# Optimization experiments

Hardware: AMD Instinct MI355X
Metric: run time of the kernel (lower is better)

The kernel has to match this reference:

```python
import jax, jax.numpy as jnp
import numpy as np

N = 1 << 20          # query points
IN_DIMS = 32
HIDDEN = 64
N_INNER = 4          # n_hidden_layers - 1 hidden->hidden layers
OUT_DIMS = 3


def _kaiming(key, shape):
    fan_in = shape[-1]
    bound = np.sqrt(6.0 / fan_in)  # kaiming_uniform with relu gain sqrt(2): sqrt(6/fan_in)
    return jax.random.uniform(key, shape, jnp.float32, -bound, bound)


def setup_inputs() -> dict:
    key = jax.random.key(0)
    ks = jax.random.split(key, 4)
    x = jax.random.normal(ks[0], (N, IN_DIMS), jnp.float32)
    W_in = _kaiming(ks[1], (HIDDEN, IN_DIMS))
    b_in = jnp.zeros((HIDDEN,), jnp.float32)
    W_hid = _kaiming(ks[2], (N_INNER, HIDDEN, HIDDEN))
    b_hid = jnp.zeros((N_INNER, HIDDEN), jnp.float32)
    W_out = _kaiming(ks[3], (OUT_DIMS, HIDDEN))
    b_out = jnp.zeros((OUT_DIMS,), jnp.float32)
    return {"x": x, "W_in": W_in, "b_in": b_in, "W_hid": W_hid,
            "b_hid": b_hid, "W_out": W_out, "b_out": b_out}


def reference(x, W_in, b_in, W_hid, b_hid, W_out, b_out):
    # torch nn.Linear: y = x @ W.T + b
    h = jax.nn.relu(x @ W_in.T + b_in)                     # [N, HIDDEN]

    def step(h, wb):
        W, b = wb
        return jax.nn.relu(h @ W.T + b), None

    h, _ = jax.lax.scan(step, h, (W_hid, b_hid))           # 4 hidden layers
    out = h @ W_out.T + b_out                              # [N, OUT_DIMS]
    return jax.nn.sigmoid(out)                             # output_activation='Sigmoid'
```

## Files before the change

### kernel.cpp

```cpp
#include <hip/hip_runtime.h>
#include <hip/hip_bf16.h>


typedef __attribute__((ext_vector_type(8))) short bf16x8;
typedef __attribute__((ext_vector_type(4))) float f32x4;

#define NFRAG 59
#define IMG_U4 (NFRAG * 64)

__device__ __forceinline__ unsigned cvtpk(float lo, float hi) {
    unsigned r;
    asm("v_cvt_pk_bf16_f32 %0, %1, %2" : "=v"(r) : "v"(lo), "v"(hi));
    return r;
}

__device__ __forceinline__ int pinv(int s) {
    return ((s >> 5) & 1) * 32 + ((s >> 2) & 1) * 16 + ((s >> 3) & 3) * 4 + (s & 3);
}

__device__ uint4 frag_value(int F, int lane,
        const float* __restrict__ W_in,  const float* __restrict__ b_in,
        const float* __restrict__ W_hid, const float* __restrict__ b_hid,
        const float* __restrict__ W_out, const float* __restrict__ b_out) {
    const int j = lane & 15, g = lane >> 4;
    uint4 r = {0u, 0u, 0u, 0u};
    if (F < 4) {
        const float* row = W_in + (F * 16 + j) * 32 + 8 * g;
        r.x = cvtpk(row[0], row[1]); r.y = cvtpk(row[2], row[3]);
        r.z = cvtpk(row[4], row[5]); r.w = cvtpk(row[6], row[7]);
    } else if (F < 36) {
        int q = F - 4, L = q >> 3, nt = (q >> 1) & 3, f = q & 1;
        const float* row = W_hid + (L * 64 + nt * 16 + j) * 64;
        int s0 = 32 * f + 8 * g;
        r.x = cvtpk(row[pinv(s0 + 0)], row[pinv(s0 + 1)]);
        r.y = cvtpk(row[pinv(s0 + 2)], row[pinv(s0 + 3)]);
        r.z = cvtpk(row[pinv(s0 + 4)], row[pinv(s0 + 5)]);
        r.w = cvtpk(row[pinv(s0 + 6)], row[pinv(s0 + 7)]);
    } else if (F < 38) {
        int f = F - 36;
        if (j < 3) {
            const float* row = W_out + j * 64;
            int s0 = 32 * f + 8 * g;
            r.x = cvtpk(row[pinv(s0 + 0)], row[pinv(s0 + 1)]);
            r.y = cvtpk(row[pinv(s0 + 2)], row[pinv(s0 + 3)]);
            r.z = cvtpk(row[pinv(s0 + 4)], row[pinv(s0 + 5)]);
            r.w = cvtpk(row[pinv(s0 + 6)], row[pinv(s0 + 7)]);
        }
    } else {
        union { uint4 u; float f[4]; } t;
        if (F < 42) {
            int nt = F - 38;
#pragma unroll
            for (int rr = 0; rr < 4; ++rr) t.f[rr] = b_in[nt * 16 + 4 * g + rr];
        } else if (F < 58) {
            int q = F - 42, L = q >> 2, nt = q & 3;
#pragma unroll
            for (int rr = 0; rr < 4; ++rr) t.f[rr] = b_hid[L * 64 + nt * 16 + 4 * g + rr];
        } else {
#pragma unroll
            for (int rr = 0; rr < 4; ++rr) t.f[rr] = (4 * g + rr < 3) ? b_out[4 * g + rr] : 0.f;
        }
        r = t.u;
    }
    return r;
}

__global__ void prep_kernel(const float* __restrict__ W_in,  const float* __restrict__ b_in,
                            const float* __restrict__ W_hid, const float* __restrict__ b_hid,
                            const float* __restrict__ W_out, const float* __restrict__ b_out,
                            uint4* __restrict__ img) {
    img[blockIdx.x * 64 + threadIdx.x] =
        frag_value(blockIdx.x, threadIdx.x, W_in, b_in, W_hid, b_hid, W_out, b_out);
}

__device__ __forceinline__ void relu_pack(const f32x4 a[4], bf16x8 h[2]) {
#pragma unroll
    for (int f = 0; f < 2; ++f) {
        union { bf16x8 v; unsigned u[4]; } t;
        t.u[0] = cvtpk(fmaxf(a[2 * f][0], 0.f), fmaxf(a[2 * f][1], 0.f));
        t.u[1] = cvtpk(fmaxf(a[2 * f][2], 0.f), fmaxf(a[2 * f][3], 0.f));
        t.u[2] = cvtpk(fmaxf(a[2 * f + 1][0], 0.f), fmaxf(a[2 * f + 1][1], 0.f));
        t.u[3] = cvtpk(fmaxf(a[2 * f + 1][2], 0.f), fmaxf(a[2 * f + 1][3], 0.f));
        h[f] = t.v;
    }
}

#define MFMA(a, b, c) __builtin_amdgcn_mfma_f32_16x16x32_bf16((a), (b), (c), 0, 0, 0)

template<bool FAST>
__global__ __launch_bounds__(512, 2) void mlp_kernel(
        const float* __restrict__ x, const uint4* __restrict__ img,
        const float* __restrict__ gW_in,  const float* __restrict__ gb_in,
        const float* __restrict__ gW_hid, const float* __restrict__ gb_hid,
        const float* __restrict__ gW_out, const float* __restrict__ gb_out,
        float* __restrict__ out) {
    __shared__ uint4 simg[IMG_U4];
    const int tid = threadIdx.x;

    if (FAST) {
#pragma unroll
        for (int i = 0; i < 8; ++i) {
            int idx = tid + i * 512;
            if (idx < IMG_U4) simg[idx] = img[idx];
        }
    } else {
        for (int idx = tid; idx < IMG_U4; idx += 512)
            simg[idx] = frag_value(idx >> 6, idx & 63,
                                   gW_in, gb_in, gW_hid, gb_hid, gW_out, gb_out);
    }
    __syncthreads();

    const int wave = tid >> 6, lane = tid & 63;
    const int j = lane & 15, g = lane >> 4;
    const uint4* lp = &simg[lane];

    const int base = (blockIdx.x * 8 + wave) * 256;

    f32x4 xrA0, xrA1, xrB0, xrB1;
    {
        const float* p = x + (size_t)(base + j) * 32 + 8 * g;
        xrA0 = *(const f32x4*)p;         xrA1 = *(const f32x4*)(p + 4);
        xrB0 = *(const f32x4*)(p + 512); xrB1 = *(const f32x4*)(p + 516);
    }

#pragma unroll 1
    for (int it = 0; it < 8; ++it) {
        const int p0 = base + it * 32;

        union { bf16x8 v; unsigned u[4]; } xA, xB;
        xA.u[0] = cvtpk(xrA0[0], xrA0[1]); xA.u[1] = cvtpk(xrA0[2], xrA0[3]);
        xA.u[2] = cvtpk(xrA1[0], xrA1[1]); xA.u[3] = cvtpk(xrA1[2], xrA1[3]);
        xB.u[0] = cvtpk(xrB0[0], xrB0[1]); xB.u[1] = cvtpk(xrB0[2], xrB0[3]);
        xB.u[2] = cvtpk(xrB1[0], xrB1[1]); xB.u[3] = cvtpk(xrB1[2], xrB1[3]);

        {
            const int pn = (it < 7) ? p0 + 32 : p0;
            const float* p = x + (size_t)(pn + j) * 32 + 8 * g;
            xrA0 = *(const f32x4*)p;         xrA1 = *(const f32x4*)(p + 4);
            xrB0 = *(const f32x4*)(p + 512); xrB1 = *(const f32x4*)(p + 516);
        }

        f32x4 aA[4], aB[4];
#pragma unroll
        for (int nt = 0; nt < 4; ++nt) {
            bf16x8 w  = *(const bf16x8*)&lp[nt * 64];
            f32x4  bz = *(const f32x4*)&lp[(38 + nt) * 64];
            aA[nt] = MFMA(w, xA.v, bz);
            aB[nt] = MFMA(w, xB.v, bz);
        }
        bf16x8 hA[2], hB[2];
        relu_pack(aA, hA); relu_pack(aB, hB);

#pragma unroll 1
        for (int L = 0; L < 4; ++L) {
            const int wb = (4 + L * 8) * 64;
            const int bb = (42 + L * 4) * 64;
            bf16x8 w0[4], w1[4]; f32x4 bz[4];
#pragma unroll
            for (int nt = 0; nt < 4; ++nt) {
                w0[nt] = *(const bf16x8*)&lp[wb + (2 * nt) * 64];
                w1[nt] = *(const bf16x8*)&lp[wb + (2 * nt + 1) * 64];
                bz[nt] = *(const f32x4*)&lp[bb + nt * 64];
            }
#pragma unroll
            for (int nt = 0; nt < 4; ++nt) {
                aA[nt] = MFMA(w0[nt], hA[0], bz[nt]);
                aB[nt] = MFMA(w0[nt], hB[0], bz[nt]);
            }
#pragma unroll
            for (int nt = 0; nt < 4; ++nt) {
                aA[nt] = MFMA(w1[nt], hA[1], aA[nt]);
                aB[nt] = MFMA(w1[nt], hB[1], aB[nt]);
            }
            relu_pack(aA, hA); relu_pack(aB, hB);
        }

        bf16x8 wo0 = *(const bf16x8*)&lp[36 * 64];
        bf16x8 wo1 = *(const bf16x8*)&lp[37 * 64];
        f32x4  bo  = *(const f32x4*)&lp[58 * 64];
        f32x4 zA = MFMA(wo0, hA[0], bo); zA = MFMA(wo1, hA[1], zA);
        f32x4 zB = MFMA(wo0, hB[0], bo); zB = MFMA(wo1, hB[1], zB);

        if (g == 0) {
            float* oA = out + (size_t)(p0 + j) * 3;
            float* oB = out + (size_t)(p0 + 16 + j) * 3;
#pragma unroll
            for (int r = 0; r < 3; ++r) {
                oA[r] = __builtin_amdgcn_rcpf(1.f + __expf(-zA[r]));
                oB[r] = __builtin_amdgcn_rcpf(1.f + __expf(-zB[r]));
            }
        }
    }
}

extern "C" void kernel_launch(void* const* d_in, const int* in_sizes, int n_in,
                              void* d_out, int out_size, void* d_ws, size_t ws_size,
                              hipStream_t stream) {
    const float* x     = (const float*)d_in[0];
    const float* W_in  = (const float*)d_in[1];
    const float* b_in  = (const float*)d_in[2];
    const float* W_hid = (const float*)d_in[3];
    const float* b_hid = (const float*)d_in[4];
    const float* W_out = (const float*)d_in[5];
    const float* b_out = (const float*)d_in[6];
    float* out = (float*)d_out;

    int n = in_sizes[0] / 32;
    int nblocks = n / 2048;

    if (ws_size >= (size_t)IMG_U4 * 16) {
        hipLaunchKernelGGL(prep_kernel, dim3(NFRAG), dim3(64), 0, stream,
                           W_in, b_in, W_hid, b_hid, W_out, b_out, (uint4*)d_ws);
        hipLaunchKernelGGL((mlp_kernel<true>), dim3(nblocks), dim3(512), 0, stream,
                           x, (const uint4*)d_ws,
                           W_in, b_in, W_hid, b_hid, W_out, b_out, out);
    } else {
        hipLaunchKernelGGL((mlp_kernel<false>), dim3(nblocks), dim3(512), 0, stream,
                           x, (const uint4*)d_ws,
                           W_in, b_in, W_hid, b_hid, W_out, b_out, out);
    }
}
```

Before: 57.02 us.

## Process four 16-point tiles per wave iteration and raise occupancy to four blocks

Each wave now handles 64 points per iteration (four MFMA column tiles) instead of 32, with the hidden-layer loop fully unrolled and processed in pairs. This reuses each loaded weight fragment across more MFMAs and gives more independent MFMA chains to hide latency. The x prefetch for the first tile is issued before the shared-memory barrier, the next tile's prefetch is moved later, and launch bounds now request 4 blocks per CU, which limits registers while the per-thread state has grown. Output stores are packed into 12-byte structs.

```diff
diff --git a/kernel.cpp b/kernel.cpp
--- a/kernel.cpp
+++ b/kernel.cpp
@@ -7,6 +7,8 @@
 
 #define NFRAG 59
 #define IMG_U4 (NFRAG * 64)
+
+struct F3 { float a, b, c; };
 
 __device__ __forceinline__ unsigned cvtpk(float lo, float hi) {
     unsigned r;
@@ -88,7 +90,7 @@
 #define MFMA(a, b, c) __builtin_amdgcn_mfma_f32_16x16x32_bf16((a), (b), (c), 0, 0, 0)
 
 template<bool FAST>
-__global__ __launch_bounds__(512, 2) void mlp_kernel(
+__global__ __launch_bounds__(512, 4) void mlp_kernel(
         const float* __restrict__ x, const uint4* __restrict__ img,
         const float* __restrict__ gW_in,  const float* __restrict__ gb_in,
         const float* __restrict__ gW_hid, const float* __restrict__ gb_hid,
@@ -108,50 +110,55 @@
             simg[idx] = frag_value(idx >> 6, idx & 63,
                                    gW_in, gb_in, gW_hid, gb_hid, gW_out, gb_out);
     }
-    __syncthreads();
 
     const int wave = tid >> 6, lane = tid & 63;
     const int j = lane & 15, g = lane >> 4;
+    const int base = (blockIdx.x * 8 + wave) * 256;
+
+    f32x4 raw[4][2];
+    {
+        const float* xp = x + (size_t)(base + j) * 32 + 8 * g;
+#pragma unroll
+        for (int t = 0; t < 4; ++t) {
+            raw[t][0] = *(const f32x4*)(xp + t * 512);
+            raw[t][1] = *(const f32x4*)(xp + t * 512 + 4);
+        }
+    }
+    __syncthreads();
+
     const uint4* lp = &simg[lane];
 
-    const int base = (blockIdx.x * 8 + wave) * 256;
-
-    f32x4 xrA0, xrA1, xrB0, xrB1;
-    {
-        const float* p = x + (size_t)(base + j) * 32 + 8 * g;
-        xrA0 = *(const f32x4*)p;         xrA1 = *(const f32x4*)(p + 4);
-        xrB0 = *(const f32x4*)(p + 512); xrB1 = *(const f32x4*)(p + 516);
-    }
-
 #pragma unroll 1
-    for (int it = 0; it < 8; ++it) {
-        const int p0 = base + it * 32;
-
-        union { bf16x8 v; unsigned u[4]; } xA, xB;
-        xA.u[0] = cvtpk(xrA0[0], xrA0[1]); xA.u[1] = cvtpk(xrA0[2], xrA0[3]);
-        xA.u[2] = cvtpk(xrA1[0], xrA1[1]); xA.u[3] = cvtpk(xrA1[2], xrA1[3]);
-        xB.u[0] = cvtpk(xrB0[0], xrB0[1]); xB.u[1] = cvtpk(xrB0[2], xrB0[3]);
-        xB.u[2] = cvtpk(xrB1[0], xrB1[1]); xB.u[3] = cvtpk(xrB1[2], xrB1[3]);
-
+    for (int it = 0; it < 4; ++it) {
+        const int p0 = base + it * 64;
+
+        bf16x8 xf[4];
+#pragma unroll
+        for (int t = 0; t < 4; ++t) {
+            union { bf16x8 v; unsigned u[4]; } a;
+            a.u[0] = cvtpk(raw[t][0][0], raw[t][0][1]);
+            a.u[1] = cvtpk(raw[t][0][2], raw[t][0][3]);
+            a.u[2] = cvtpk(raw[t][1][0], raw[t][1][1]);
+            a.u[3] = cvtpk(raw[t][1][2], raw[t][1][3]);
+            xf[t] = a.v;
+        }
+
+        bf16x8 hfrag[4][2];
         {
-            const int pn = (it < 7) ? p0 + 32 : p0;
-            const float* p = x + (size_t)(pn + j) * 32 + 8 * g;
-            xrA0 = *(const f32x4*)p;         xrA1 = *(const f32x4*)(p + 4);
-            xrB0 = *(const f32x4*)(p + 512); xrB1 = *(const f32x4*)(p + 516);
-        }
-
-        f32x4 aA[4], aB[4];
-#pragma unroll
-        for (int nt = 0; nt < 4; ++nt) {
-            bf16x8 w  = *(const bf16x8*)&lp[nt * 64];
-            f32x4  bz = *(const f32x4*)&lp[(38 + nt) * 64];
-            aA[nt] = MFMA(w, xA.v, bz);
-            aB[nt] = MFMA(w, xB.v, bz);
-        }
-        bf16x8 hA[2], hB[2];
-        relu_pack(aA, hA); relu_pack(aB, hB);
-
-#pragma unroll 1
+            f32x4 acc[4][4];
+#pragma unroll
+            for (int nt = 0; nt < 4; ++nt) {
+                bf16x8 w  = *(const bf16x8*)&lp[nt * 64];
+                f32x4  bz = *(const f32x4*)&lp[(38 + nt) * 64];
+#pragma unroll
+                for (int t = 0; t < 4; ++t)
+                    acc[t][nt] = MFMA(w, xf[t], bz);
+            }
+#pragma unroll
+            for (int t = 0; t < 4; ++t) relu_pack(acc[t], hfrag[t]);
+        }
+
+#pragma unroll
         for (int L = 0; L < 4; ++L) {
             const int wb = (4 + L * 8) * 64;
             const int bb = (42 + L * 4) * 64;
@@ -163,31 +170,52 @@
                 bz[nt] = *(const f32x4*)&lp[bb + nt * 64];
             }
 #pragma unroll
-            for (int nt = 0; nt < 4; ++nt) {
-                aA[nt] = MFMA(w0[nt], hA[0], bz[nt]);
-                aB[nt] = MFMA(w0[nt], hB[0], bz[nt]);
-            }
-#pragma unroll
-            for (int nt = 0; nt < 4; ++nt) {
-                aA[nt] = MFMA(w1[nt], hA[1], aA[nt]);
-                aB[nt] = MFMA(w1[nt], hB[1], aB[nt]);
-            }
-            relu_pack(aA, hA); relu_pack(aB, hB);
+            for (int pr = 0; pr < 2; ++pr) {
+                f32x4 pa[2][4];
+#pragma unroll
+                for (int q = 0; q < 2; ++q)
+#pragma unroll
+                    for (int nt = 0; nt < 4; ++nt)
+                        pa[q][nt] = MFMA(w0[nt], hfrag[2 * pr + q][0], bz[nt]);
+#pragma unroll
+                for (int q = 0; q < 2; ++q)
+#pragma unroll
+                    for (int nt = 0; nt < 4; ++nt)
+                        pa[q][nt] = MFMA(w1[nt], hfrag[2 * pr + q][1], pa[q][nt]);
+#pragma unroll
+                for (int q = 0; q < 2; ++q) relu_pack(pa[q], hfrag[2 * pr + q]);
+            }
         }
 
         bf16x8 wo0 = *(const bf16x8*)&lp[36 * 64];
         bf16x8 wo1 = *(const bf16x8*)&lp[37 * 64];
         f32x4  bo  = *(const f32x4*)&lp[58 * 64];
-        f32x4 zA = MFMA(wo0, hA[0], bo); zA = MFMA(wo1, hA[1], zA);
-        f32x4 zB = MFMA(wo0, hB[0], bo); zB = MFMA(wo1, hB[1], zB);
+        f32x4 z[4];
+#pragma unroll
+        for (int t = 0; t < 4; ++t) {
+            f32x4 tmp = MFMA(wo0, hfrag[t][0], bo);
+            z[t] = MFMA(wo1, hfrag[t][1], tmp);
+        }
+
+        {
+            const int pn = (it < 3) ? p0 + 64 : p0;
+            const float* xp = x + (size_t)(pn + j) * 32 + 8 * g;
+#pragma unroll
+            for (int t = 0; t < 4; ++t) {
+                raw[t][0] = *(const f32x4*)(xp + t * 512);
+                raw[t][1] = *(const f32x4*)(xp + t * 512 + 4);
+            }
+        }
 
         if (g == 0) {
-            float* oA = out + (size_t)(p0 + j) * 3;
-            float* oB = out + (size_t)(p0 + 16 + j) * 3;
-#pragma unroll
-            for (int r = 0; r < 3; ++r) {
-                oA[r] = __builtin_amdgcn_rcpf(1.f + __expf(-zA[r]));
-                oB[r] = __builtin_amdgcn_rcpf(1.f + __expf(-zB[r]));
+            float* ob = out + (size_t)(p0 + j) * 3;
+#pragma unroll
+            for (int t = 0; t < 4; ++t) {
+                F3 v;
+                v.a = __builtin_amdgcn_rcpf(1.f + __expf(-z[t][0]));
+                v.b = __builtin_amdgcn_rcpf(1.f + __expf(-z[t][1]));
+                v.c = __builtin_amdgcn_rcpf(1.f + __expf(-z[t][2]));
+                *(F3*)(ob + t * 48) = v;
             }
         }
     }
```

New measurement: 57.59 us. About the same (+1.0%).
